# Kernel tuning notes

Measured on AMD Instinct MI355X. Metric: run time of the kernel, lower is better.

## Reference

```python
import jax, jax.numpy as jnp
import numpy as np
import math

D_MODEL = 1024
N_HEADS = 16
DK = D_MODEL // N_HEADS


def setup_inputs() -> dict:
    key = jax.random.key(0)
    kx, kqkv, kproj = jax.random.split(key, 3)
    B, T = 4, 2048
    x = jax.random.normal(kx, (B, T, D_MODEL), dtype=jnp.float32)
    # torch Linear weight is [out, in]; y = x @ W.T
    W_qkv = jax.random.normal(kqkv, (3 * D_MODEL, D_MODEL), dtype=jnp.float32) * (1.0 / math.sqrt(D_MODEL))
    W_proj = jax.random.normal(kproj, (D_MODEL, D_MODEL), dtype=jnp.float32) * (1.0 / math.sqrt(D_MODEL))
    return {"x": x, "W_qkv": W_qkv, "W_proj": W_proj}


def reference(x, W_qkv, W_proj):
    B, T, D = x.shape
    qkv = jnp.einsum("btd,ed->bte", x, W_qkv)  # [B,T,3D]
    q, k, v = jnp.split(qkv, 3, axis=-1)
    # [B,T,D] -> [B,H,T,dk]
    def heads(t):
        return t.reshape(B, T, N_HEADS, DK).transpose(0, 2, 1, 3)
    q, k, v = heads(q), heads(k), heads(v)
    scale = 1.0 / math.sqrt(DK)
    att = jnp.einsum("bhqd,bhkd->bhqk", q, k) * scale  # [B,H,T,T]
    att = jax.nn.softmax(att, axis=-1)
    out = jnp.einsum("bhqk,bhkd->bhqd", att, v)  # [B,H,T,dk]
    out = out.transpose(0, 2, 1, 3).reshape(B, T, D)
    return jnp.einsum("btd,ed->bte", out, W_proj)
```

## Files before the change

kernel.cpp:

```cpp
#include <hip/hip_runtime.h>
#include <hip/hip_bf16.h>

#define D_MODEL 1024
#define N_HEADS 16
#define DK 64
#define B_SZ 4
#define T_SEQ 2048
#define M_ROWS (B_SZ * T_SEQ)
#define QK_SCALE_LOG2 0.18033688f

#define XN ((size_t)M_ROWS * D_MODEL)
#define WQ ((size_t)3 * D_MODEL * D_MODEL)
#define WP ((size_t)D_MODEL * D_MODEL)

typedef short bf16x8 __attribute__((ext_vector_type(8)));
typedef float f32x4  __attribute__((ext_vector_type(4)));

__device__ inline unsigned short f32_to_bf16(float f) {
    union { float f; unsigned int u; } v; v.f = f;
    unsigned int r = v.u + 0x7fff + ((v.u >> 16) & 1);
    return (unsigned short)(r >> 16);
}
__device__ inline unsigned int pack_bf16x2(float a, float b) {
    __hip_bfloat162 t = __float22bfloat162_rn(make_float2(a, b));
    union { __hip_bfloat162 v; unsigned int u; } c; c.v = t;
    return c.u;
}

__global__ __launch_bounds__(256) void cast_all(
    const float* __restrict__ x, const float* __restrict__ W_qkv,
    const float* __restrict__ W_proj,
    unsigned short* __restrict__ xb, unsigned short* __restrict__ wqb,
    unsigned short* __restrict__ wpb)
{
    const size_t total = (XN + WQ + WP) / 4;
    for (size_t i4 = blockIdx.x * 256 + threadIdx.x; i4 < total;
         i4 += gridDim.x * 256) {
        const size_t i = i4 * 4;
        const float* src; unsigned short* dst; float sc = 1.0f; size_t off;
        if (i < XN) {
            src = x; dst = xb; off = i;
        } else if (i < XN + WQ) {
            off = i - XN; src = W_qkv; dst = wqb;
            if (off < (size_t)D_MODEL * D_MODEL) sc = QK_SCALE_LOG2;
        } else {
            off = i - XN - WQ; src = W_proj; dst = wpb;
        }
        float4 v = *(const float4*)(src + off);
        ushort4 h;
        h.x = f32_to_bf16(v.x * sc); h.y = f32_to_bf16(v.y * sc);
        h.z = f32_to_bf16(v.z * sc); h.w = f32_to_bf16(v.w * sc);
        *(ushort4*)(dst + off) = h;
    }
}

template <typename OutT, bool FUSE_VT>
__global__ __launch_bounds__(256, 4) void gemm_bf16_nt(
    const unsigned short* __restrict__ A, const unsigned short* __restrict__ B,
    OutT* __restrict__ C, unsigned short* __restrict__ vt,
    int M, int N, int K)
{
    __shared__ __align__(16) unsigned short sA[2][128 * 64];
    __shared__ __align__(16) unsigned short sB[2][128 * 64];

    const int t    = threadIdx.x;
    const int wave = t >> 6;
    const int lane = t & 63;
    const int l15  = lane & 15;
    const int quad = lane >> 4;
    const int swz  = l15 & 7;

    const int cpx = gridDim.x >> 3;
    const int wg  = (blockIdx.x & 7) * cpx + (blockIdx.x >> 3);
    const int nbx = N >> 7;
    const int n0  = (wg % nbx) * 128;
    const int m0  = (wg / nbx) * 128;

    const unsigned short* gplane = (wave < 2) ? A : B;
    unsigned short* lplane = (wave < 2) ? sA[0] : sB[0];
    const int row0 = ((wave < 2) ? m0 : n0) + (wave & 1) * 64;
    const int loff = (wave & 1) * 4096;
    const int rsub = lane >> 3;
    const int cg   = (lane & 7) ^ rsub;
    const unsigned short* gbase =
        gplane + (size_t)(row0 + rsub) * K + cg * 8;

    f32x4 acc[4][4];
#pragma unroll
    for (int i = 0; i < 4; ++i)
#pragma unroll
        for (int j = 0; j < 4; ++j) acc[i][j] = (f32x4){0.f, 0.f, 0.f, 0.f};

    const int wr = (wave >> 1) * 64;
    const int wc = (wave & 1) * 64;

    const int nk = K >> 6;
#pragma unroll
    for (int i = 0; i < 8; ++i) {
        __builtin_amdgcn_global_load_lds(
            (const __attribute__((address_space(1))) unsigned int*)
                (gbase + (size_t)(i * 8) * K),
            (__attribute__((address_space(3))) unsigned int*)
                (lplane + loff + i * 512),
            16, 0, 0);
    }

    for (int kt = 0; kt < nk; ++kt) {
        __syncthreads();

        if (kt + 1 < nk) {
            const int k0n = (kt + 1) << 6;
            const int nb  = (kt + 1) & 1;
#pragma unroll
            for (int i = 0; i < 8; ++i) {
                __builtin_amdgcn_global_load_lds(
                    (const __attribute__((address_space(1))) unsigned int*)
                        (gbase + k0n + (size_t)(i * 8) * K),
                    (__attribute__((address_space(3))) unsigned int*)
                        (lplane + nb * 8192 + loff + i * 512),
                    16, 0, 0);
            }
        }

        const int cb = kt & 1;
#pragma unroll
        for (int kk = 0; kk < 2; ++kk) {
            bf16x8 a[4], b[4];
            const int ch = kk * 4 + quad;
            const int co = (ch ^ swz) * 8;
#pragma unroll
            for (int f = 0; f < 4; ++f) {
                a[f] = *(const bf16x8*)&sA[cb][(wr + f * 16 + l15) * 64 + co];
                b[f] = *(const bf16x8*)&sB[cb][(wc + f * 16 + l15) * 64 + co];
            }
            __builtin_amdgcn_s_setprio(1);
#pragma unroll
            for (int mi = 0; mi < 4; ++mi)
#pragma unroll
                for (int ni = 0; ni < 4; ++ni)
                    acc[mi][ni] = __builtin_amdgcn_mfma_f32_16x16x32_bf16(
                        a[mi], b[ni], acc[mi][ni], 0, 0, 0);
            __builtin_amdgcn_s_setprio(0);
        }
    }

    if constexpr (FUSE_VT) {
        if (n0 >= 2 * D_MODEL) {
            const int bb   = m0 >> 11;
            const int tile = (m0 & 2047) >> 7;
            const int hA   = (n0 + wc - 2 * D_MODEL) >> 6;
            unsigned short* vtile =
                vt + ((size_t)((bb * N_HEADS + hA) * (T_SEQ / 128) + tile))
                     * (16 * 64 * 8);
            const int chi = (wr >> 6) * 8;
#pragma unroll
            for (int cc = 0; cc < 2; ++cc) {
                const int c   = chi + cc * 4 + quad;
                const int mi0 = 2 * cc;
#pragma unroll
                for (int ni = 0; ni < 4; ++ni) {
                    const int d = ni * 16 + l15;
                    uint4 p;
                    p.x = pack_bf16x2(acc[mi0][ni][0],     acc[mi0][ni][1]);
                    p.y = pack_bf16x2(acc[mi0][ni][2],     acc[mi0][ni][3]);
                    p.z = pack_bf16x2(acc[mi0 + 1][ni][0], acc[mi0 + 1][ni][1]);
                    p.w = pack_bf16x2(acc[mi0 + 1][ni][2], acc[mi0 + 1][ni][3]);
                    *(uint4*)(vtile + (c * 64 + d) * 8) = p;
                }
            }
            return;
        }
    }

#pragma unroll
    for (int mi = 0; mi < 4; ++mi)
#pragma unroll
        for (int r = 0; r < 4; ++r) {
            OutT* crow =
                C + (size_t)(m0 + wr + mi * 16 + quad * 4 + r) * N + n0 + wc + l15;
#pragma unroll
            for (int ni = 0; ni < 4; ++ni) {
                if constexpr (sizeof(OutT) == 2)
                    crow[ni * 16] = (OutT)f32_to_bf16(acc[mi][ni][r]);
                else
                    crow[ni * 16] = (OutT)acc[mi][ni][r];
            }
        }
}

__global__ __launch_bounds__(256, 4) void attn_mfma(
    const unsigned short* __restrict__ qkvb,
    const unsigned short* __restrict__ vt,
    unsigned short* __restrict__ ob)
{
    __shared__ __align__(16) unsigned short Ksw[2][128 * 64];

    const int t    = threadIdx.x;
    const int wave = t >> 6;
    const int lane = t & 63;
    const int l15  = t & 15;
    const int quad = lane >> 4;
    const int swz  = l15 & 7;

    const int b  = blockIdx.z;
    const int h  = blockIdx.y;
    const int q0 = blockIdx.x * 128;

    bf16x8 qa[2][2];
#pragma unroll
    for (int qs = 0; qs < 2; ++qs) {
        const unsigned short* qrow =
            qkvb + ((size_t)(b * T_SEQ) + q0 + wave * 32 + qs * 16 + l15)
                   * (3 * D_MODEL) + h * DK;
        qa[qs][0] = *(const bf16x8*)(qrow + quad * 8);
        qa[qs][1] = *(const bf16x8*)(qrow + 32 + quad * 8);
    }

    f32x4 O[2][4], Lacc[2];
#pragma unroll
    for (int qs = 0; qs < 2; ++qs) {
        Lacc[qs] = (f32x4){0.f, 0.f, 0.f, 0.f};
#pragma unroll
        for (int nd = 0; nd < 4; ++nd) O[qs][nd] = (f32x4){0.f, 0.f, 0.f, 0.f};
    }

    const short one_bf = (short)0x3F80;
    const bf16x8 ones8 = {one_bf, one_bf, one_bf, one_bf,
                          one_bf, one_bf, one_bf, one_bf};

    const unsigned short* kbase =
        qkvb + (size_t)(b * T_SEQ) * (3 * D_MODEL) + D_MODEL + h * DK;
    const unsigned short* vbase =
        vt + (size_t)(b * N_HEADS + h) * DK * T_SEQ;

    const int krl  = wave * 32 + (lane >> 3);
    const int kcol = ((lane & 7) ^ (lane >> 3)) * 8;

#pragma unroll
    for (int i = 0; i < 4; ++i) {
        const int rk = krl + i * 8;
        __builtin_amdgcn_global_load_lds(
            (const __attribute__((address_space(1))) unsigned int*)
                (kbase + (size_t)rk * (3 * D_MODEL) + kcol),
            (__attribute__((address_space(3))) unsigned int*)
                (&Ksw[0][(wave * 4 + i) * 512]),
            16, 0, 0);
    }

    const int NT = T_SEQ / 128;
    for (int tile = 0; tile < NT; ++tile) {
        __syncthreads();

        if (tile + 1 < NT) {
            const int c0n = (tile + 1) * 128;
            const int nb  = (tile + 1) & 1;
#pragma unroll
            for (int i = 0; i < 4; ++i) {
                const int rk = krl + i * 8;
                __builtin_amdgcn_global_load_lds(
                    (const __attribute__((address_space(1))) unsigned int*)
                        (kbase + (size_t)(c0n + rk) * (3 * D_MODEL) + kcol),
                    (__attribute__((address_space(3))) unsigned int*)
                        (&Ksw[nb][(wave * 4 + i) * 512]),
                    16, 0, 0);
            }
        }

        const int cb = tile & 1;
        const unsigned short* vtile = vbase + (size_t)tile * (16 * 64 * 8);
        const unsigned short* vlane = vtile + quad * 512 + l15 * 8;
#pragma unroll
        for (int half = 0; half < 2; ++half) {
            f32x4 S[2][4];
#pragma unroll
            for (int qs = 0; qs < 2; ++qs)
#pragma unroll
                for (int nf = 0; nf < 4; ++nf) S[qs][nf] = (f32x4){0.f, 0.f, 0.f, 0.f};

            __builtin_amdgcn_s_setprio(1);
#pragma unroll
            for (int ks = 0; ks < 2; ++ks) {
                const int ch = ks * 4 + quad;
#pragma unroll
                for (int nf = 0; nf < 4; ++nf) {
                    const int row = half * 64 + nf * 16 + l15;
                    const bf16x8 kf =
                        *(const bf16x8*)&Ksw[cb][row * 64 + ((ch ^ swz) * 8)];
                    S[0][nf] = __builtin_amdgcn_mfma_f32_16x16x32_bf16(
                        kf, qa[0][ks], S[0][nf], 0, 0, 0);
                    S[1][nf] = __builtin_amdgcn_mfma_f32_16x16x32_bf16(
                        kf, qa[1][ks], S[1][nf], 0, 0, 0);
                }
            }
            __builtin_amdgcn_s_setprio(0);

#pragma unroll
            for (int gl = 0; gl < 2; ++gl) {
                bf16x8 pf[2];
#pragma unroll
                for (int qs = 0; qs < 2; ++qs) {
                    union { uint4 u; bf16x8 v; } cv;
                    const f32x4 s0 = S[qs][2 * gl];
                    const f32x4 s1 = S[qs][2 * gl + 1];
                    cv.u.x = pack_bf16x2(__builtin_amdgcn_exp2f(s0[0]),
                                         __builtin_amdgcn_exp2f(s0[1]));
                    cv.u.y = pack_bf16x2(__builtin_amdgcn_exp2f(s0[2]),
                                         __builtin_amdgcn_exp2f(s0[3]));
                    cv.u.z = pack_bf16x2(__builtin_amdgcn_exp2f(s1[0]),
                                         __builtin_amdgcn_exp2f(s1[1]));
                    cv.u.w = pack_bf16x2(__builtin_amdgcn_exp2f(s1[2]),
                                         __builtin_amdgcn_exp2f(s1[3]));
                    pf[qs] = cv.v;
                }
                const int g = half * 2 + gl;
                const unsigned short* vptr = vlane + (size_t)g * 2048;
                __builtin_amdgcn_s_setprio(1);
#pragma unroll
                for (int nd = 0; nd < 4; ++nd) {
                    const bf16x8 vb = *(const bf16x8*)(vptr + nd * 128);
                    O[0][nd] = __builtin_amdgcn_mfma_f32_16x16x32_bf16(
                        pf[0], vb, O[0][nd], 0, 0, 0);
                    O[1][nd] = __builtin_amdgcn_mfma_f32_16x16x32_bf16(
                        pf[1], vb, O[1][nd], 0, 0, 0);
                }
                Lacc[0] = __builtin_amdgcn_mfma_f32_16x16x32_bf16(
                    pf[0], ones8, Lacc[0], 0, 0, 0);
                Lacc[1] = __builtin_amdgcn_mfma_f32_16x16x32_bf16(
                    pf[1], ones8, Lacc[1], 0, 0, 0);
                __builtin_amdgcn_s_setprio(0);
            }
        }
    }

#pragma unroll
    for (int qs = 0; qs < 2; ++qs)
#pragma unroll
        for (int r = 0; r < 4; ++r) {
            const float invl = 1.0f / Lacc[qs][r];
            const size_t rowbase =
                ((size_t)(b * T_SEQ) + q0 + wave * 32 + qs * 16 + quad * 4 + r)
                * D_MODEL + h * DK + l15;
#pragma unroll
            for (int nd = 0; nd < 4; ++nd)
                ob[rowbase + nd * 16] = f32_to_bf16(O[qs][nd][r] * invl);
        }
}

extern "C" void kernel_launch(void* const* d_in, const int* in_sizes, int n_in,
                              void* d_out, int out_size, void* d_ws, size_t ws_size,
                              hipStream_t stream)
{
    const float* x      = (const float*)d_in[0];
    const float* W_qkv  = (const float*)d_in[1];
    const float* W_proj = (const float*)d_in[2];
    float* out = (float*)d_out;

    unsigned short* xb   = (unsigned short*)d_ws;
    unsigned short* wqb  = xb + XN;
    unsigned short* wpb  = wqb + WQ;
    unsigned short* qkvb = wpb + WP;
    unsigned short* vtb  = qkvb + (size_t)M_ROWS * 3 * D_MODEL;
    unsigned short* ab   = xb;

    dim3 blk(256);
    cast_all<<<1024, blk, 0, stream>>>(x, W_qkv, W_proj, xb, wqb, wpb);

    gemm_bf16_nt<unsigned short, true>
        <<<dim3((3 * D_MODEL / 128) * (M_ROWS / 128)), blk, 0, stream>>>(
        xb, wqb, qkvb, vtb, M_ROWS, 3 * D_MODEL, D_MODEL);

    attn_mfma<<<dim3(T_SEQ / 128, N_HEADS, B_SZ), blk, 0, stream>>>(
        qkvb, vtb, ab);

    gemm_bf16_nt<float, false>
        <<<dim3((D_MODEL / 128) * (M_ROWS / 128)), blk, 0, stream>>>(
        ab, wpb, out, nullptr, M_ROWS, D_MODEL, D_MODEL);
}
```

Before: 247.2 us.

## Pre-swizzle weights into fragment layout and load B operand directly from global

```diff
diff --git a/kernel.cpp b/kernel.cpp
--- a/kernel.cpp
+++ b/kernel.cpp
@@ -33,35 +33,51 @@
     unsigned short* __restrict__ xb, unsigned short* __restrict__ wqb,
     unsigned short* __restrict__ wpb)
 {
-    const size_t total = (XN + WQ + WP) / 4;
-    for (size_t i4 = blockIdx.x * 256 + threadIdx.x; i4 < total;
-         i4 += gridDim.x * 256) {
-        const size_t i = i4 * 4;
-        const float* src; unsigned short* dst; float sc = 1.0f; size_t off;
-        if (i < XN) {
-            src = x; dst = xb; off = i;
-        } else if (i < XN + WQ) {
-            off = i - XN; src = W_qkv; dst = wqb;
-            if (off < (size_t)D_MODEL * D_MODEL) sc = QK_SCALE_LOG2;
+    const size_t NX4 = XN / 4;
+    const size_t NQ8 = WQ / 8;
+    const size_t NP8 = WP / 8;
+    const size_t total = NX4 + NQ8 + NP8;
+    for (size_t idx = blockIdx.x * 256 + threadIdx.x; idx < total;
+         idx += gridDim.x * 256) {
+        if (idx < NX4) {
+            const size_t off = idx * 4;
+            float4 v = *(const float4*)(x + off);
+            ushort4 h;
+            h.x = f32_to_bf16(v.x); h.y = f32_to_bf16(v.y);
+            h.z = f32_to_bf16(v.z); h.w = f32_to_bf16(v.w);
+            *(ushort4*)(xb + off) = h;
         } else {
-            off = i - XN - WQ; src = W_proj; dst = wpb;
-        }
-        float4 v = *(const float4*)(src + off);
-        ushort4 h;
-        h.x = f32_to_bf16(v.x * sc); h.y = f32_to_bf16(v.y * sc);
-        h.z = f32_to_bf16(v.z * sc); h.w = f32_to_bf16(v.w * sc);
-        *(ushort4*)(dst + off) = h;
+            const float* src; unsigned short* dst; size_t j; float sc = 1.0f;
+            if (idx < NX4 + NQ8) {
+                j = idx - NX4; src = W_qkv; dst = wqb;
+                if ((j >> 7) < (size_t)D_MODEL) sc = QK_SCALE_LOG2;
+            } else {
+                j = idx - NX4 - NQ8; src = W_proj; dst = wpb;
+            }
+            const int n  = (int)(j >> 7);
+            const int k8 = (int)(j & 127);
+            const float* s = src + ((size_t)n << 10) + (k8 << 3);
+            float4 v0 = *(const float4*)(s);
+            float4 v1 = *(const float4*)(s + 4);
+            union { unsigned short h[8]; uint4 u; } o;
+            o.h[0] = f32_to_bf16(v0.x * sc); o.h[1] = f32_to_bf16(v0.y * sc);
+            o.h[2] = f32_to_bf16(v0.z * sc); o.h[3] = f32_to_bf16(v0.w * sc);
+            o.h[4] = f32_to_bf16(v1.x * sc); o.h[5] = f32_to_bf16(v1.y * sc);
+            o.h[6] = f32_to_bf16(v1.z * sc); o.h[7] = f32_to_bf16(v1.w * sc);
+            unsigned short* d =
+                dst + ((((size_t)(n >> 7) * 128 + k8) * 128 + (n & 127)) << 3);
+            *(uint4*)d = o.u;
+        }
     }
 }
 
 template <typename OutT, bool FUSE_VT>
-__global__ __launch_bounds__(256, 4) void gemm_bf16_nt(
-    const unsigned short* __restrict__ A, const unsigned short* __restrict__ B,
+__global__ __launch_bounds__(256, 3) void gemm_bf16_nt(
+    const unsigned short* __restrict__ A, const unsigned short* __restrict__ Bf,
     OutT* __restrict__ C, unsigned short* __restrict__ vt,
     int M, int N, int K)
 {
     __shared__ __align__(16) unsigned short sA[2][128 * 64];
-    __shared__ __align__(16) unsigned short sB[2][128 * 64];
 
     const int t    = threadIdx.x;
     const int wave = t >> 6;
@@ -72,52 +88,57 @@
 
     const int cpx = gridDim.x >> 3;
     const int wg  = (blockIdx.x & 7) * cpx + (blockIdx.x >> 3);
-    const int nbx = N >> 7;
-    const int n0  = (wg % nbx) * 128;
-    const int m0  = (wg / nbx) * 128;
-
-    const unsigned short* gplane = (wave < 2) ? A : B;
-    unsigned short* lplane = (wave < 2) ? sA[0] : sB[0];
-    const int row0 = ((wave < 2) ? m0 : n0) + (wave & 1) * 64;
-    const int loff = (wave & 1) * 4096;
+    const int nbm = M >> 7;
+    const int n0  = (wg / nbm) * 128;
+    const int m0  = (wg % nbm) * 128;
+
     const int rsub = lane >> 3;
     const int cg   = (lane & 7) ^ rsub;
     const unsigned short* gbase =
-        gplane + (size_t)(row0 + rsub) * K + cg * 8;
-
-    f32x4 acc[4][4];
-#pragma unroll
-    for (int i = 0; i < 4; ++i)
-#pragma unroll
-        for (int j = 0; j < 4; ++j) acc[i][j] = (f32x4){0.f, 0.f, 0.f, 0.f};
+        A + (size_t)(m0 + wave * 32 + rsub) * K + cg * 8;
 
     const int wr = (wave >> 1) * 64;
     const int wc = (wave & 1) * 64;
+    const unsigned short* bfb =
+        Bf + (((size_t)(n0 >> 7) * 128) * 128 + wc + l15) * 8;
+
+    f32x4 acc[4][4];
+#pragma unroll
+    for (int i = 0; i < 4; ++i)
+#pragma unroll
+        for (int j = 0; j < 4; ++j) acc[i][j] = (f32x4){0.f, 0.f, 0.f, 0.f};
 
     const int nk = K >> 6;
 #pragma unroll
-    for (int i = 0; i < 8; ++i) {
+    for (int i = 0; i < 4; ++i) {
         __builtin_amdgcn_global_load_lds(
             (const __attribute__((address_space(1))) unsigned int*)
                 (gbase + (size_t)(i * 8) * K),
             (__attribute__((address_space(3))) unsigned int*)
-                (lplane + loff + i * 512),
+                (&sA[0][wave * 2048 + i * 512]),
             16, 0, 0);
     }
 
     for (int kt = 0; kt < nk; ++kt) {
         __syncthreads();
+
+        const unsigned short* bk = bfb + (size_t)(kt * 8 + quad) * 1024;
+        bf16x8 b0[4], b1[4];
+#pragma unroll
+        for (int f = 0; f < 4; ++f) b0[f] = *(const bf16x8*)(bk + f * 128);
+#pragma unroll
+        for (int f = 0; f < 4; ++f) b1[f] = *(const bf16x8*)(bk + 4096 + f * 128);
 
         if (kt + 1 < nk) {
             const int k0n = (kt + 1) << 6;
             const int nb  = (kt + 1) & 1;
 #pragma unroll
-            for (int i = 0; i < 8; ++i) {
+            for (int i = 0; i < 4; ++i) {
                 __builtin_amdgcn_global_load_lds(
                     (const __attribute__((address_space(1))) unsigned int*)
                         (gbase + k0n + (size_t)(i * 8) * K),
                     (__attribute__((address_space(3))) unsigned int*)
-                        (lplane + nb * 8192 + loff + i * 512),
+                        (&sA[nb][wave * 2048 + i * 512]),
                     16, 0, 0);
             }
         }
@@ -125,21 +146,19 @@
         const int cb = kt & 1;
 #pragma unroll
         for (int kk = 0; kk < 2; ++kk) {
-            bf16x8 a[4], b[4];
+            bf16x8 a[4];
             const int ch = kk * 4 + quad;
             const int co = (ch ^ swz) * 8;
 #pragma unroll
-            for (int f = 0; f < 4; ++f) {
+            for (int f = 0; f < 4; ++f)
                 a[f] = *(const bf16x8*)&sA[cb][(wr + f * 16 + l15) * 64 + co];
-                b[f] = *(const bf16x8*)&sB[cb][(wc + f * 16 + l15) * 64 + co];
-            }
             __builtin_amdgcn_s_setprio(1);
 #pragma unroll
             for (int mi = 0; mi < 4; ++mi)
 #pragma unroll
                 for (int ni = 0; ni < 4; ++ni)
                     acc[mi][ni] = __builtin_amdgcn_mfma_f32_16x16x32_bf16(
-                        a[mi], b[ni], acc[mi][ni], 0, 0, 0);
+                        a[mi], (kk ? b1 : b0)[ni], acc[mi][ni], 0, 0, 0);
             __builtin_amdgcn_s_setprio(0);
         }
     }
```

After: 272.9 us. 1.1x slower.
